# Kernel tuning notes

Hardware: AMD Instinct MI355X
Metric: run time of the kernel (lower is better)

The kernel has to match this reference:

```python
import jax, jax.numpy as jnp
import numpy as np


def setup_inputs() -> dict:
    key = jax.random.key(0)
    k1, k2 = jax.random.split(key)
    B, L, H = 32, 256, 512
    encoder_hidden_states = jax.random.normal(k1, (B, L, H), dtype=jnp.float32)
    durations_gt = jax.random.randint(k2, (B, L), 0, 16, dtype=jnp.int32)
    return {"encoder_hidden_states": encoder_hidden_states, "durations_gt": durations_gt}


def reference(encoder_hidden_states, durations_gt):
    # Length regulator: out[b, t] = x[b, i] where i is the phoneme whose
    # cumulative-duration bucket contains frame t; zero-padded past the
    # row's total duration. Equivalent to per-row repeat_interleave + pad,
    # but expressed as a single vectorized searchsorted + gather.
    x = encoder_hidden_states
    B, L, H = x.shape
    csum = jnp.cumsum(durations_gt, axis=1)          # [B, L]
    total = csum[:, -1]                              # [B] real expanded lengths
    T = int(jnp.max(total))                          # max_durations (concrete)
    t = jnp.arange(T, dtype=csum.dtype)              # [T]
    # idx[b, t] = searchsorted(csum[b], t, side='right')
    idx = jax.vmap(lambda c: jnp.searchsorted(c, t, side='right'))(csum)  # [B, T]
    idx = jnp.clip(idx, 0, L - 1)
    outputs = jnp.take_along_axis(x, idx[:, :, None], axis=1)  # [B, T, H]
    encoder_masks = (t[None, :] < total[:, None]).astype(jnp.int32)  # [B, T]
    outputs = outputs * encoder_masks[:, :, None].astype(x.dtype)   # zero pad region
    return outputs, encoder_masks
```

## Files before the change

kernel.cpp:

```cpp
#include <hip/hip_runtime.h>

constexpr int B = 32;
constexpr int L = 256;
constexpr int H = 512;
constexpr int HV = H / 4;

__global__ void duration_scan_kernel(const int* __restrict__ dur,
                                     int* __restrict__ csum) {
    __shared__ int s[L];
    const int b = blockIdx.x;
    const int i = threadIdx.x;
    s[i] = dur[b * L + i];
    __syncthreads();
    #pragma unroll
    for (int off = 1; off < L; off <<= 1) {
        int t = (i >= off) ? s[i - off] : 0;
        __syncthreads();
        s[i] += t;
        __syncthreads();
    }
    csum[b * L + i] = s[i];
}

__global__ void expand_kernel(const float4* __restrict__ x,
                              const int* __restrict__ csum,
                              float4* __restrict__ out,
                              float* __restrict__ mask,
                              int T) {
    __shared__ int sc[L];
    const int b = blockIdx.y;
    const int t = blockIdx.x;
    const int tid = threadIdx.x;

    sc[tid] = csum[b * L + tid];
    sc[tid + 128] = csum[b * L + tid + 128];
    __syncthreads();

    const int total = sc[L - 1];

    int lo = 0, hi = L;
    while (lo < hi) {
        int mid = (lo + hi) >> 1;
        if (sc[mid] <= t) lo = mid + 1; else hi = mid;
    }
    const int idx = (lo < L - 1) ? lo : (L - 1);

    float4 val;
    if (t < total) {
        val = x[((size_t)(b * L + idx)) * HV + tid];
    } else {
        val = make_float4(0.f, 0.f, 0.f, 0.f);
    }
    out[((size_t)b * T + t) * HV + tid] = val;

    if (tid == 0) {
        mask[(size_t)b * T + t] = (t < total) ? 1.0f : 0.0f;
    }
}

extern "C" void kernel_launch(void* const* d_in, const int* in_sizes, int n_in,
                              void* d_out, int out_size, void* d_ws, size_t ws_size,
                              hipStream_t stream) {
    const float* x = (const float*)d_in[0];
    const int* dur = (const int*)d_in[1];
    float* out = (float*)d_out;

    const int T = out_size / (B * (H + 1));

    int* csum = (int*)d_ws;

    duration_scan_kernel<<<B, L, 0, stream>>>(dur, csum);

    float* mask_out = out + (size_t)B * T * H;
    dim3 grid(T, B);
    expand_kernel<<<grid, 128, 0, stream>>>((const float4*)x, csum,
                                            (float4*)out, mask_out, T);
}
```

Baseline: 174.4 us.

## Fuse duration scan into expand kernel and process frame chunks per block

Drops the separate cumulative-sum kernel and its workspace round trip. Each block now recomputes the prefix sum of one batch row in shared memory and then expands a chunk of 16 frames with 256 threads, advancing the phoneme index incrementally instead of doing a binary search per frame. This removes one launch and cuts the block count, at the cost of repeating the scan in every block. Output copying now loops over frames within a block.

```diff
diff --git a/kernel.cpp b/kernel.cpp
--- a/kernel.cpp
+++ b/kernel.cpp
@@ -4,57 +4,60 @@
 constexpr int L = 256;
 constexpr int H = 512;
 constexpr int HV = H / 4;
+constexpr int CHUNK = 16;
 
-__global__ void duration_scan_kernel(const int* __restrict__ dur,
-                                     int* __restrict__ csum) {
-    __shared__ int s[L];
-    const int b = blockIdx.x;
-    const int i = threadIdx.x;
-    s[i] = dur[b * L + i];
+__global__ __launch_bounds__(256) void lr_fused_kernel(
+    const float4* __restrict__ x,
+    const int* __restrict__ dur,
+    float4* __restrict__ out,
+    float* __restrict__ mask,
+    int T) {
+    __shared__ int sc[L];
+    const int b = blockIdx.y;
+    const int tid = threadIdx.x;
+
+    sc[tid] = dur[b * L + tid];
     __syncthreads();
     #pragma unroll
     for (int off = 1; off < L; off <<= 1) {
-        int t = (i >= off) ? s[i - off] : 0;
+        int t = (tid >= off) ? sc[tid - off] : 0;
         __syncthreads();
-        s[i] += t;
+        sc[tid] += t;
         __syncthreads();
     }
-    csum[b * L + i] = s[i];
-}
-
-__global__ void expand_kernel(const float4* __restrict__ x,
-                              const int* __restrict__ csum,
-                              float4* __restrict__ out,
-                              float* __restrict__ mask,
-                              int T) {
-    __shared__ int sc[L];
-    const int b = blockIdx.y;
-    const int t = blockIdx.x;
-    const int tid = threadIdx.x;
-
-    sc[tid] = csum[b * L + tid];
-    sc[tid + 128] = csum[b * L + tid + 128];
-    __syncthreads();
-
     const int total = sc[L - 1];
 
+    const int t0 = blockIdx.x * CHUNK;
+    const int half = tid >> 7;
+    const int lane = tid & 127;
+
+    const int tfirst = t0 + half;
     int lo = 0, hi = L;
     while (lo < hi) {
         int mid = (lo + hi) >> 1;
-        if (sc[mid] <= t) lo = mid + 1; else hi = mid;
+        if (sc[mid] <= tfirst) lo = mid + 1; else hi = mid;
     }
-    const int idx = (lo < L - 1) ? lo : (L - 1);
+    int idx = lo;
 
-    float4 val;
-    if (t < total) {
-        val = x[((size_t)(b * L + idx)) * HV + tid];
-    } else {
-        val = make_float4(0.f, 0.f, 0.f, 0.f);
+    #pragma unroll
+    for (int i = 0; i < CHUNK / 2; ++i) {
+        const int t = t0 + 2 * i + half;
+        while (idx < L && sc[idx] <= t) ++idx;
+        const int gidx = (idx < L - 1) ? idx : (L - 1);
+        if (t < T) {
+            float4 val = make_float4(0.f, 0.f, 0.f, 0.f);
+            if (t < total) {
+                val = x[((size_t)(b * L + gidx)) * HV + lane];
+            }
+            out[((size_t)b * T + t) * HV + lane] = val;
+        }
     }
-    out[((size_t)b * T + t) * HV + tid] = val;
 
-    if (tid == 0) {
-        mask[(size_t)b * T + t] = (t < total) ? 1.0f : 0.0f;
+    if (tid < CHUNK) {
+        const int t = t0 + tid;
+        if (t < T) {
+            mask[(size_t)b * T + t] = (t < total) ? 1.0f : 0.0f;
+        }
     }
 }
 
@@ -67,12 +70,8 @@
 
     const int T = out_size / (B * (H + 1));
 
-    int* csum = (int*)d_ws;
-
-    duration_scan_kernel<<<B, L, 0, stream>>>(dur, csum);
-
     float* mask_out = out + (size_t)B * T * H;
-    dim3 grid(T, B);
-    expand_kernel<<<grid, 128, 0, stream>>>((const float4*)x, csum,
-                                            (float4*)out, mask_out, T);
+    dim3 grid((T + CHUNK - 1) / CHUNK, B);
+    lr_fused_kernel<<<grid, 256, 0, stream>>>((const float4*)x, dur,
+                                              (float4*)out, mask_out, T);
 }
```

New measurement: 154.8 us (median of 2 runs). 1.13x faster.
